# Kernel tuning notes

Measured on AMD Instinct MI355X. Metric: run time of the kernel, lower is better.

## Reference

```python
import jax, jax.numpy as jnp
import numpy as np

C = 64  # in_channels == out_channels (required by final view)

def setup_inputs() -> dict:
    key = jax.random.key(0)
    ks = jax.random.split(key, 7)
    x = jax.random.normal(ks[0], (2, C, 16, 16, 16), dtype=jnp.float32)
    s = 1.0 / np.sqrt(C)
    Wq = jax.random.uniform(ks[1], (C, C), jnp.float32, -s, s)
    bq = jax.random.uniform(ks[2], (C,), jnp.float32, -s, s)
    Wk = jax.random.uniform(ks[3], (C, C), jnp.float32, -s, s)
    bk = jax.random.uniform(ks[4], (C,), jnp.float32, -s, s)
    Wv = jax.random.uniform(ks[5], (C, C), jnp.float32, -s, s)
    bv = jax.random.uniform(ks[6], (C,), jnp.float32, -s, s)
    return {"x": x, "Wq": Wq, "bq": bq, "Wk": Wk, "bk": bk, "Wv": Wv, "bv": bv}

def _proj(x, W, b):
    # 1x1x1 Conv3d == per-voxel channel GEMM; x: [B,C,D,H,W]
    return jnp.einsum('oc,bcdhw->bodhw', W, x) + b[None, :, None, None, None]

def reference(x, Wq, bq, Wk, bk, Wv, bv):
    B, Cin, D, H, W = x.shape
    q = _proj(x, Wq, bq).reshape(B, C, -1)  # [B,C,N]
    k = _proj(x, Wk, bk).reshape(B, C, -1)
    v = _proj(x, Wv, bv).reshape(B, C, -1)
    # attention[b,i,j] = softmax_j(q_i . k_j); NOTE: unscaled, as in the source
    attn = jax.nn.softmax(jnp.einsum('bci,bcj->bij', q, k), axis=-1)
    out = jnp.einsum('bcj,bij->bci', v, attn)  # out_i = sum_j a_ij v_j
    return out.reshape(x.shape)
```

## Files before the change

### kernel.cpp

```cpp
#include <hip/hip_runtime.h>
#include <math.h>

#define CCH 64
#define NVOX 4096
#define NB 2
#define RS 72

typedef _Float16 f16x8 __attribute__((ext_vector_type(8)));
typedef _Float16 f16x4 __attribute__((ext_vector_type(4)));
typedef __fp16   g16x2 __attribute__((ext_vector_type(2)));
typedef float f32x4 __attribute__((ext_vector_type(4)));

__global__ __launch_bounds__(256) void qkv_proj(
    const float* __restrict__ x,
    const float* __restrict__ Wq, const float* __restrict__ bq,
    const float* __restrict__ Wk, const float* __restrict__ bk,
    const float* __restrict__ Wv, const float* __restrict__ bv,
    _Float16* __restrict__ qh, _Float16* __restrict__ kh, _Float16* __restrict__ vh)
{
    __shared__ float Ws[3 * 64 * 64];
    __shared__ float xs[64 * 32];
    const int t  = threadIdx.x;
    const int b  = blockIdx.x >> 7;
    const int i0 = (blockIdx.x & 127) * 32;

    {
        const float4* Wq4 = (const float4*)Wq;
        const float4* Wk4 = (const float4*)Wk;
        const float4* Wv4 = (const float4*)Wv;
        float4* Ws4 = (float4*)Ws;
#pragma unroll
        for (int s = 0; s < 4; ++s) {
            int idx = t + 256 * s;
            Ws4[idx]        = Wq4[idx];
            Ws4[1024 + idx] = Wk4[idx];
            Ws4[2048 + idx] = Wv4[idx];
        }
    }
    {
        int cc = t >> 2;
        int m0 = (t & 3) * 8;
        const float* src = x + ((b * CCH + cc) * NVOX) + i0 + m0;
#pragma unroll
        for (int s = 0; s < 8; ++s) xs[cc * 32 + m0 + s] = src[s];
    }
    __syncthreads();

    const int vox = t & 31;
    const int c0  = (t >> 5) * 8;

#pragma unroll
    for (int m = 0; m < 3; ++m) {
        const float* Wm  = &Ws[m * 4096];
        const float* bia = (m == 0) ? bq : (m == 1) ? bk : bv;
        float acc[8];
#pragma unroll
        for (int j = 0; j < 8; ++j) acc[j] = bia[c0 + j];
        for (int cc = 0; cc < 64; cc += 4) {
            float xv0 = xs[(cc + 0) * 32 + vox];
            float xv1 = xs[(cc + 1) * 32 + vox];
            float xv2 = xs[(cc + 2) * 32 + vox];
            float xv3 = xs[(cc + 3) * 32 + vox];
#pragma unroll
            for (int j = 0; j < 8; ++j) {
                float4 w = *(const float4*)&Wm[(c0 + j) * 64 + cc];
                acc[j] = fmaf(w.x, xv0, acc[j]);
                acc[j] = fmaf(w.y, xv1, acc[j]);
                acc[j] = fmaf(w.z, xv2, acc[j]);
                acc[j] = fmaf(w.w, xv3, acc[j]);
            }
        }
        if (m < 2) {
            f16x8 hv;
#pragma unroll
            for (int j = 0; j < 8; ++j) hv[j] = (_Float16)acc[j];
            _Float16* dst = ((m == 0) ? qh : kh) + ((b * NVOX) + i0 + vox) * CCH + c0;
            *(f16x8*)dst = hv;
        } else {
#pragma unroll
            for (int j = 0; j < 8; ++j)
                vh[(b * CCH + c0 + j) * NVOX + i0 + vox] = (_Float16)acc[j];
        }
    }
}

template <int SPLIT>
__global__ __launch_bounds__(256) void attn(
    const _Float16* __restrict__ qh, const _Float16* __restrict__ kh,
    const _Float16* __restrict__ vh,
    _Float16* __restrict__ po,
    float* __restrict__ ml,
    float* __restrict__ out)
{
    __shared__ _Float16 ksl[2][64 * RS];
    __shared__ _Float16 vsl[2][64 * RS];

    constexpr int LS = (SPLIT == 8) ? 3 : (SPLIT == 4) ? 2 : (SPLIT == 2) ? 1 : 0;
    const int t    = threadIdx.x;
    const int h    = blockIdx.x & (SPLIT - 1);
    const int tile = blockIdx.x >> LS;
    const int b    = tile >> 6;
    const int i0   = (tile & 63) * 64;

    const int lane = t & 63;
    const int w    = t >> 6;
    const int q4   = lane >> 4;
    const int n    = lane & 15;

    const int row = t >> 2;
    const int c0  = (t & 3) * 16;
    const int JT  = 64 / SPLIT;

    auto load_tile = [&](int jt, float4 r[4]) {
        const int j0 = (h * JT + jt) * 64;
        const float4* ks = (const float4*)&kh[((size_t)(b * NVOX) + j0 + row) * CCH + c0];
        r[0] = ks[0]; r[1] = ks[1];
        const float4* vs = (const float4*)&vh[((size_t)b * CCH + row) * NVOX + j0 + c0];
        r[2] = vs[0]; r[3] = vs[1];
    };
    auto store_tile = [&](int buf, const float4 r[4]) {
        *(float4*)&ksl[buf][row * RS + c0]     = r[0];
        *(float4*)&ksl[buf][row * RS + c0 + 8] = r[1];
        *(float4*)&vsl[buf][row * RS + c0]     = r[2];
        *(float4*)&vsl[buf][row * RS + c0 + 8] = r[3];
    };

    f16x8 aq[2];
    {
        const _Float16* qrow = qh + ((size_t)(b * NVOX) + i0 + w * 16 + n) * CCH + q4 * 8;
        aq[0] = *(const f16x8*)(qrow);
        aq[1] = *(const f16x8*)(qrow + 32);
    }

    float4 stg[4];
    load_tile(0, stg);
    store_tile(0, stg);

    float m_prev = -1e30f, l = 0.f;
    f32x4 o[4];
#pragma unroll
    for (int mt = 0; mt < 4; ++mt) o[mt] = (f32x4){0.f, 0.f, 0.f, 0.f};

    __syncthreads();

    for (int jt = 0; jt < JT; ++jt) {
        const int buf = jt & 1;
        if (jt + 1 < JT) load_tile(jt + 1, stg);

        f32x4 s[4];
#pragma unroll
        for (int nt = 0; nt < 4; ++nt) s[nt] = (f32x4){0.f, 0.f, 0.f, 0.f};
#pragma unroll
        for (int ks = 0; ks < 2; ++ks) {
#pragma unroll
            for (int nt = 0; nt < 4; ++nt) {
                f16x8 ak = *(const f16x8*)&ksl[buf][(nt * 16 + n) * RS + ks * 32 + q4 * 8];
                s[nt] = __builtin_amdgcn_mfma_f32_16x16x32_f16(ak, aq[ks], s[nt], 0, 0, 0);
            }
        }

        float mx = -1e30f;
#pragma unroll
        for (int nt = 0; nt < 4; ++nt)
#pragma unroll
            for (int r = 0; r < 4; ++r) mx = fmaxf(mx, s[nt][r]);
        mx = fmaxf(mx, __shfl_xor(mx, 16, 64));
        mx = fmaxf(mx, __shfl_xor(mx, 32, 64));
        const float mn = fmaxf(m_prev, mx);

        float p[4][4], sum = 0.f;
#pragma unroll
        for (int nt = 0; nt < 4; ++nt)
#pragma unroll
            for (int r = 0; r < 4; ++r) {
                p[nt][r] = __expf(s[nt][r] - mn);
                sum += p[nt][r];
            }
        sum += __shfl_xor(sum, 16, 64);
        sum += __shfl_xor(sum, 32, 64);

        const float alpha = __expf(m_prev - mn);
        l = l * alpha + sum;
        m_prev = mn;

#pragma unroll
        for (int mt = 0; mt < 4; ++mt)
#pragma unroll
            for (int r = 0; r < 4; ++r) o[mt][r] *= alpha;

        f16x4 bp[4];
#pragma unroll
        for (int nt = 0; nt < 4; ++nt) {
            union { g16x2 g2[2]; f16x4 h4; } u;
            u.g2[0] = __builtin_amdgcn_cvt_pkrtz(p[nt][0], p[nt][1]);
            u.g2[1] = __builtin_amdgcn_cvt_pkrtz(p[nt][2], p[nt][3]);
            bp[nt] = u.h4;
        }

#pragma unroll
        for (int nt = 0; nt < 4; ++nt) {
#pragma unroll
            for (int mt = 0; mt < 4; ++mt) {
                f16x4 av = *(const f16x4*)&vsl[buf][(mt * 16 + n) * RS + nt * 16 + q4 * 4];
                o[mt] = __builtin_amdgcn_mfma_f32_16x16x16f16(av, bp[nt], o[mt], 0, 0, 0);
            }
        }

        if (jt + 1 < JT) {
            __syncthreads();
            store_tile(buf ^ 1, stg);
            __syncthreads();
        }
    }

    const int ig = i0 + w * 16 + n;
    if (SPLIT > 1) {
        const size_t base = ((size_t)(b * SPLIT + h) * 64) * NVOX;
#pragma unroll
        for (int mt = 0; mt < 4; ++mt)
#pragma unroll
            for (int r = 0; r < 4; ++r)
                po[base + (size_t)(mt * 16 + q4 * 4 + r) * NVOX + ig] = (_Float16)o[mt][r];
        if (q4 == 0) {
            float2* mlp = (float2*)&ml[((size_t)(b * SPLIT + h) * NVOX + ig) * 2];
            *mlp = make_float2(m_prev, l);
        }
    } else {
        const float inv = 1.0f / l;
#pragma unroll
        for (int mt = 0; mt < 4; ++mt)
#pragma unroll
            for (int r = 0; r < 4; ++r)
                out[(size_t)(b * CCH + mt * 16 + q4 * 4 + r) * NVOX + ig] = o[mt][r] * inv;
    }
}

template <int SPLIT>
__global__ __launch_bounds__(256) void combine(
    const _Float16* __restrict__ po, const float* __restrict__ ml,
    float* __restrict__ out)
{
    __shared__ float wls[SPLIT * 64];
    const int t  = threadIdx.x;
    const int b  = blockIdx.x >> 6;
    const int i0 = (blockIdx.x & 63) * 64;

    if (t < 64) {
        const int i = i0 + t;
        float mv[SPLIT], lv[SPLIT], M = -1e30f;
#pragma unroll
        for (int h = 0; h < SPLIT; ++h) {
            mv[h] = ml[((size_t)(b * SPLIT + h) * NVOX + i) * 2 + 0];
            lv[h] = ml[((size_t)(b * SPLIT + h) * NVOX + i) * 2 + 1];
            M = fmaxf(M, mv[h]);
        }
        float den = 0.f;
#pragma unroll
        for (int h = 0; h < SPLIT; ++h) den += lv[h] * __expf(mv[h] - M);
        const float inv = 1.0f / den;
#pragma unroll
        for (int h = 0; h < SPLIT; ++h) wls[h * 64 + t] = __expf(mv[h] - M) * inv;
    }
    __syncthreads();

    const int c  = t >> 2;
    const int iq = t & 3;
    float acc[16];
#pragma unroll
    for (int u = 0; u < 16; ++u) acc[u] = 0.f;
#pragma unroll
    for (int h = 0; h < SPLIT; ++h) {
        const f16x8* src = (const f16x8*)&po[((size_t)(b * SPLIT + h) * 64 + c) * NVOX + i0 + iq * 16];
        const float* wp  = &wls[h * 64 + iq * 16];
#pragma unroll
        for (int u = 0; u < 2; ++u) {
            f16x8 f = src[u];
#pragma unroll
            for (int e = 0; e < 8; ++e)
                acc[u * 8 + e] = fmaf((float)f[e], wp[u * 8 + e], acc[u * 8 + e]);
        }
    }
    float4* dst = (float4*)&out[(size_t)(b * CCH + c) * NVOX + i0 + iq * 16];
#pragma unroll
    for (int u = 0; u < 4; ++u)
        dst[u] = make_float4(acc[u * 4], acc[u * 4 + 1], acc[u * 4 + 2], acc[u * 4 + 3]);
}

extern "C" void kernel_launch(void* const* d_in, const int* in_sizes, int n_in,
                              void* d_out, int out_size, void* d_ws, size_t ws_size,
                              hipStream_t stream)
{
    const float* x  = (const float*)d_in[0];
    const float* Wq = (const float*)d_in[1];
    const float* bq = (const float*)d_in[2];
    const float* Wk = (const float*)d_in[3];
    const float* bk = (const float*)d_in[4];
    const float* Wv = (const float*)d_in[5];
    const float* bv = (const float*)d_in[6];
    float* out = (float*)d_out;

    _Float16* qh = (_Float16*)d_ws;
    _Float16* kh = qh + NB * NVOX * CCH;
    _Float16* vh = kh + NB * NVOX * CCH;
    _Float16* po = vh + NB * NVOX * CCH;
    const size_t qkv_bytes = (size_t)3 * NB * NVOX * CCH * sizeof(_Float16);

    qkv_proj<<<NB * (NVOX / 32), 256, 0, stream>>>(x, Wq, bq, Wk, bk, Wv, bv, qh, kh, vh);

    const size_t need8 = qkv_bytes +
        (size_t)NB * 8 * 64 * NVOX * sizeof(_Float16) + (size_t)NB * 8 * NVOX * 2 * sizeof(float);
    const size_t need4 = qkv_bytes +
        (size_t)NB * 4 * 64 * NVOX * sizeof(_Float16) + (size_t)NB * 4 * NVOX * 2 * sizeof(float);
    const size_t need2 = qkv_bytes +
        (size_t)NB * 2 * 64 * NVOX * sizeof(_Float16) + (size_t)NB * 2 * NVOX * 2 * sizeof(float);

    if (ws_size >= need8) {
        float* ml = (float*)(po + (size_t)NB * 8 * 64 * NVOX);
        attn<8><<<NB * 64 * 8, 256, 0, stream>>>(qh, kh, vh, po, ml, out);
        combine<8><<<NB * 64, 256, 0, stream>>>(po, ml, out);
    } else if (ws_size >= need4) {
        float* ml = (float*)(po + (size_t)NB * 4 * 64 * NVOX);
        attn<4><<<NB * 64 * 4, 256, 0, stream>>>(qh, kh, vh, po, ml, out);
        combine<4><<<NB * 64, 256, 0, stream>>>(po, ml, out);
    } else if (ws_size >= need2) {
        float* ml = (float*)(po + (size_t)NB * 2 * 64 * NVOX);
        attn<2><<<NB * 64 * 2, 256, 0, stream>>>(qh, kh, vh, po, ml, out);
        combine<2><<<NB * 64, 256, 0, stream>>>(po, ml, out);
    } else {
        attn<1><<<NB * 64, 256, 0, stream>>>(qh, kh, vh, nullptr, nullptr, out);
    }
}
```

Baseline: 120.0 us.

## Process two query groups per wave to reuse K/V tiles; coalesce partial stores

Each wave now handles 32 query rows (two 16-row groups) instead of 16, so each K/V tile loaded into LDS and each K/V fragment read feeds twice as many MFMAs, halving the global and LDS traffic per query. The grid is halved to match. The split-path partial output is transposed through LDS and written with 16-byte vector stores instead of scattered half-precision stores. The cost is more registers per thread, which may lower occupancy, and fewer blocks in flight: with SPLIT=8 the grid drops from 1024 to 512 blocks on 256 CUs.

Measured after the change: 109.1 us. 9.1% less time.

```diff
diff --git a/kernel.cpp b/kernel.cpp
--- a/kernel.cpp
+++ b/kernel.cpp
@@ -5,6 +5,7 @@
 #define NVOX 4096
 #define NB 2
 #define RS 72
+#define TS 136
 
 typedef _Float16 f16x8 __attribute__((ext_vector_type(8)));
 typedef _Float16 f16x4 __attribute__((ext_vector_type(4)));
@@ -99,8 +100,8 @@
     const int t    = threadIdx.x;
     const int h    = blockIdx.x & (SPLIT - 1);
     const int tile = blockIdx.x >> LS;
-    const int b    = tile >> 6;
-    const int i0   = (tile & 63) * 64;
+    const int b    = tile >> 5;
+    const int i0   = (tile & 31) * 128;
 
     const int lane = t & 63;
     const int w    = t >> 6;
@@ -125,21 +126,25 @@
         *(float4*)&vsl[buf][row * RS + c0 + 8] = r[3];
     };
 
-    f16x8 aq[2];
-    {
-        const _Float16* qrow = qh + ((size_t)(b * NVOX) + i0 + w * 16 + n) * CCH + q4 * 8;
-        aq[0] = *(const f16x8*)(qrow);
-        aq[1] = *(const f16x8*)(qrow + 32);
+    f16x8 aq[2][2];
+#pragma unroll
+    for (int g = 0; g < 2; ++g) {
+        const _Float16* qrow =
+            qh + ((size_t)(b * NVOX) + i0 + w * 32 + g * 16 + n) * CCH + q4 * 8;
+        aq[g][0] = *(const f16x8*)(qrow);
+        aq[g][1] = *(const f16x8*)(qrow + 32);
     }
 
     float4 stg[4];
     load_tile(0, stg);
     store_tile(0, stg);
 
-    float m_prev = -1e30f, l = 0.f;
-    f32x4 o[4];
-#pragma unroll
-    for (int mt = 0; mt < 4; ++mt) o[mt] = (f32x4){0.f, 0.f, 0.f, 0.f};
+    float m_prev[2] = {-1e30f, -1e30f}, l[2] = {0.f, 0.f};
+    f32x4 o[2][4];
+#pragma unroll
+    for (int g = 0; g < 2; ++g)
+#pragma unroll
+        for (int mt = 0; mt < 4; ++mt) o[g][mt] = (f32x4){0.f, 0.f, 0.f, 0.f};
 
     __syncthreads();
 
@@ -147,62 +152,72 @@
         const int buf = jt & 1;
         if (jt + 1 < JT) load_tile(jt + 1, stg);
 
-        f32x4 s[4];
-#pragma unroll
-        for (int nt = 0; nt < 4; ++nt) s[nt] = (f32x4){0.f, 0.f, 0.f, 0.f};
+        f32x4 s[2][4];
+#pragma unroll
+        for (int g = 0; g < 2; ++g)
+#pragma unroll
+            for (int nt = 0; nt < 4; ++nt) s[g][nt] = (f32x4){0.f, 0.f, 0.f, 0.f};
 #pragma unroll
         for (int ks = 0; ks < 2; ++ks) {
 #pragma unroll
             for (int nt = 0; nt < 4; ++nt) {
                 f16x8 ak = *(const f16x8*)&ksl[buf][(nt * 16 + n) * RS + ks * 32 + q4 * 8];
-                s[nt] = __builtin_amdgcn_mfma_f32_16x16x32_f16(ak, aq[ks], s[nt], 0, 0, 0);
-            }
-        }
-
-        float mx = -1e30f;
-#pragma unroll
-        for (int nt = 0; nt < 4; ++nt)
-#pragma unroll
-            for (int r = 0; r < 4; ++r) mx = fmaxf(mx, s[nt][r]);
-        mx = fmaxf(mx, __shfl_xor(mx, 16, 64));
-        mx = fmaxf(mx, __shfl_xor(mx, 32, 64));
-        const float mn = fmaxf(m_prev, mx);
-
-        float p[4][4], sum = 0.f;
-#pragma unroll
-        for (int nt = 0; nt < 4; ++nt)
-#pragma unroll
-            for (int r = 0; r < 4; ++r) {
-                p[nt][r] = __expf(s[nt][r] - mn);
-                sum += p[nt][r];
-            }
-        sum += __shfl_xor(sum, 16, 64);
-        sum += __shfl_xor(sum, 32, 64);
-
-        const float alpha = __expf(m_prev - mn);
-        l = l * alpha + sum;
-        m_prev = mn;
-
-#pragma unroll
-        for (int mt = 0; mt < 4; ++mt)
-#pragma unroll
-            for (int r = 0; r < 4; ++r) o[mt][r] *= alpha;
-
-        f16x4 bp[4];
-#pragma unroll
-        for (int nt = 0; nt < 4; ++nt) {
-            union { g16x2 g2[2]; f16x4 h4; } u;
-            u.g2[0] = __builtin_amdgcn_cvt_pkrtz(p[nt][0], p[nt][1]);
-            u.g2[1] = __builtin_amdgcn_cvt_pkrtz(p[nt][2], p[nt][3]);
-            bp[nt] = u.h4;
-        }
+                s[0][nt] = __builtin_amdgcn_mfma_f32_16x16x32_f16(ak, aq[0][ks], s[0][nt], 0, 0, 0);
+                s[1][nt] = __builtin_amdgcn_mfma_f32_16x16x32_f16(ak, aq[1][ks], s[1][nt], 0, 0, 0);
+            }
+        }
+
+        f16x4 bp[2][4];
+        float alpha[2];
+#pragma unroll
+        for (int g = 0; g < 2; ++g) {
+            float mx = -1e30f;
+#pragma unroll
+            for (int nt = 0; nt < 4; ++nt)
+#pragma unroll
+                for (int r = 0; r < 4; ++r) mx = fmaxf(mx, s[g][nt][r]);
+            mx = fmaxf(mx, __shfl_xor(mx, 16, 64));
+            mx = fmaxf(mx, __shfl_xor(mx, 32, 64));
+            const float mn = fmaxf(m_prev[g], mx);
+
+            float p[4][4], sum = 0.f;
+#pragma unroll
+            for (int nt = 0; nt < 4; ++nt)
+#pragma unroll
+                for (int r = 0; r < 4; ++r) {
+                    p[nt][r] = __expf(s[g][nt][r] - mn);
+                    sum += p[nt][r];
+                }
+            sum += __shfl_xor(sum, 16, 64);
+            sum += __shfl_xor(sum, 32, 64);
+
+            alpha[g]  = __expf(m_prev[g] - mn);
+            l[g]      = l[g] * alpha[g] + sum;
+            m_prev[g] = mn;
+
+#pragma unroll
+            for (int nt = 0; nt < 4; ++nt) {
+                union { g16x2 g2[2]; f16x4 h4; } u;
+                u.g2[0] = __builtin_amdgcn_cvt_pkrtz(p[nt][0], p[nt][1]);
+                u.g2[1] = __builtin_amdgcn_cvt_pkrtz(p[nt][2], p[nt][3]);
+                bp[g][nt] = u.h4;
+            }
+        }
+
+#pragma unroll
+        for (int g = 0; g < 2; ++g)
+#pragma unroll
+            for (int mt = 0; mt < 4; ++mt)
+#pragma unroll
+                for (int r = 0; r < 4; ++r) o[g][mt][r] *= alpha[g];
 
 #pragma unroll
         for (int nt = 0; nt < 4; ++nt) {
 #pragma unroll
             for (int mt = 0; mt < 4; ++mt) {
                 f16x4 av = *(const f16x4*)&vsl[buf][(mt * 16 + n) * RS + nt * 16 + q4 * 4];
-                o[mt] = __builtin_amdgcn_mfma_f32_16x16x16f16(av, bp[nt], o[mt], 0, 0, 0);
+                o[0][mt] = __builtin_amdgcn_mfma_f32_16x16x16f16(av, bp[0][nt], o[0][mt], 0, 0, 0);
+                o[1][mt] = __builtin_amdgcn_mfma_f32_16x16x16f16(av, bp[1][nt], o[1][mt], 0, 0, 0);
             }
         }
 
@@ -213,25 +228,46 @@
         }
     }
 
-    const int ig = i0 + w * 16 + n;
     if (SPLIT > 1) {
-        const size_t base = ((size_t)(b * SPLIT + h) * 64) * NVOX;
-#pragma unroll
-        for (int mt = 0; mt < 4; ++mt)
-#pragma unroll
-            for (int r = 0; r < 4; ++r)
-                po[base + (size_t)(mt * 16 + q4 * 4 + r) * NVOX + ig] = (_Float16)o[mt][r];
-        if (q4 == 0) {
-            float2* mlp = (float2*)&ml[((size_t)(b * SPLIT + h) * NVOX + ig) * 2];
-            *mlp = make_float2(m_prev, l);
+        __syncthreads();
+        _Float16* tb = &ksl[0][0];
+#pragma unroll
+        for (int g = 0; g < 2; ++g)
+#pragma unroll
+            for (int mt = 0; mt < 4; ++mt)
+#pragma unroll
+                for (int r = 0; r < 4; ++r)
+                    tb[(mt * 16 + q4 * 4 + r) * TS + w * 32 + g * 16 + n] =
+                        (_Float16)o[g][mt][r];
+#pragma unroll
+        for (int g = 0; g < 2; ++g) {
+            if (q4 == 0) {
+                const int ig = i0 + w * 32 + g * 16 + n;
+                float2* mlp = (float2*)&ml[((size_t)(b * SPLIT + h) * NVOX + ig) * 2];
+                *mlp = make_float2(m_prev[g], l[g]);
+            }
+        }
+        __syncthreads();
+        const int cr = t >> 2;
+        const int ib = (t & 3) * 32;
+        const size_t base = ((size_t)(b * SPLIT + h) * 64 + cr) * NVOX + i0 + ib;
+#pragma unroll
+        for (int u = 0; u < 4; ++u) {
+            f16x8 vv = *(const f16x8*)&tb[cr * TS + ib + u * 8];
+            *(f16x8*)&po[base + u * 8] = vv;
         }
     } else {
-        const float inv = 1.0f / l;
-#pragma unroll
-        for (int mt = 0; mt < 4; ++mt)
-#pragma unroll
-            for (int r = 0; r < 4; ++r)
-                out[(size_t)(b * CCH + mt * 16 + q4 * 4 + r) * NVOX + ig] = o[mt][r] * inv;
+#pragma unroll
+        for (int g = 0; g < 2; ++g) {
+            const int ig = i0 + w * 32 + g * 16 + n;
+            const float inv = 1.0f / l[g];
+#pragma unroll
+            for (int mt = 0; mt < 4; ++mt)
+#pragma unroll
+                for (int r = 0; r < 4; ++r)
+                    out[(size_t)(b * CCH + mt * 16 + q4 * 4 + r) * NVOX + ig] =
+                        o[g][mt][r] * inv;
+        }
     }
 }
 
@@ -316,17 +352,17 @@
 
     if (ws_size >= need8) {
         float* ml = (float*)(po + (size_t)NB * 8 * 64 * NVOX);
-        attn<8><<<NB * 64 * 8, 256, 0, stream>>>(qh, kh, vh, po, ml, out);
+        attn<8><<<NB * 32 * 8, 256, 0, stream>>>(qh, kh, vh, po, ml, out);
         combine<8><<<NB * 64, 256, 0, stream>>>(po, ml, out);
     } else if (ws_size >= need4) {
         float* ml = (float*)(po + (size_t)NB * 4 * 64 * NVOX);
-        attn<4><<<NB * 64 * 4, 256, 0, stream>>>(qh, kh, vh, po, ml, out);
+        attn<4><<<NB * 32 * 4, 256, 0, stream>>>(qh, kh, vh, po, ml, out);
         combine<4><<<NB * 64, 256, 0, stream>>>(po, ml, out);
     } else if (ws_size >= need2) {
         float* ml = (float*)(po + (size_t)NB * 2 * 64 * NVOX);
-        attn<2><<<NB * 64 * 2, 256, 0, stream>>>(qh, kh, vh, po, ml, out);
+        attn<2><<<NB * 32 * 2, 256, 0, stream>>>(qh, kh, vh, po, ml, out);
         combine<2><<<NB * 64, 256, 0, stream>>>(po, ml, out);
     } else {
-        attn<1><<<NB * 64, 256, 0, stream>>>(qh, kh, vh, nullptr, nullptr, out);
+        attn<1><<<NB * 32, 256, 0, stream>>>(qh, kh, vh, nullptr, nullptr, out);
     }
 }
```
